# Optimization experiments

Measured on AMD Instinct MI355X. Metric: run time of the kernel, lower is better.

The kernel has to match this reference:

```python
import jax, jax.numpy as jnp
import numpy as np
from jax import lax

VOCAB = 32000
H = 1024
T = 4096


def setup_inputs() -> dict:
    key = jax.random.key(0)
    ks = jax.random.split(key, 6)
    s = 1.0 / np.sqrt(H)  # PyTorch GRU init scale
    x = jax.random.randint(ks[0], (T,), 0, VOCAB)
    embedding = jax.random.normal(ks[1], (VOCAB, H), dtype=jnp.float32)
    # direction 0 = 'forward', direction 1 = 'reverse' (both run left-to-right
    # here because the original feeds one timestep at a time)
    w_ih = jax.random.uniform(ks[2], (2, 3 * H, H), jnp.float32, -s, s)
    w_hh = jax.random.uniform(ks[3], (2, 3 * H, H), jnp.float32, -s, s)
    b_ih = jax.random.uniform(ks[4], (2, 3 * H), jnp.float32, -s, s)
    b_hh = jax.random.uniform(ks[5], (2, 3 * H), jnp.float32, -s, s)
    return {"x": x, "embedding": embedding, "w_ih": w_ih, "w_hh": w_hh,
            "b_ih": b_ih, "b_hh": b_hh}


def reference(x, embedding, w_ih, w_hh, b_ih, b_hh):
    emb = embedding[x]  # (T, H)
    # Precompute input-side gate projections for both directions: (T, 2, 3H)
    x_proj = jnp.einsum('th,dgh->tdg', emb, w_ih) + b_ih

    def step(h, xp):  # h: (2, H), xp: (2, 3H)
        hp = jnp.einsum('dh,dgh->dg', h, w_hh) + b_hh  # (2, 3H)
        xr, xz, xn = xp[:, :H], xp[:, H:2 * H], xp[:, 2 * H:]
        hr, hz, hn = hp[:, :H], hp[:, H:2 * H], hp[:, 2 * H:]
        r = jax.nn.sigmoid(xr + hr)
        z = jax.nn.sigmoid(xz + hz)
        n = jnp.tanh(xn + r * hn)
        h_new = (1.0 - z) * n + z * h
        return h_new, h_new

    h0 = jnp.zeros((2, H), emb.dtype)
    h_last, hs = lax.scan(step, h0, x_proj)  # hs: (T, 2, H)
    # per-step output = concat(dir0_hidden, dir1_hidden) -> (T, 2H)
    outputs = hs.reshape(T, 2 * H)
    # final hidden = sum of the two direction hiddens, shape (1, H)
    hidden = (h_last[0] + h_last[1])[None, :]
    return outputs, hidden
```

## Files before the change

kernel.cpp:

```cpp
#include <hip/hip_runtime.h>
#include <hip/hip_bf16.h>
#include <stdint.h>

#define HDIM 1024
#define TSEQ 4096
#define GATES3 3072
#define NTOT 6144

#define COMM_OFF (64u * 1024 * 1024)
#define XFIN_OFF (COMM_OFF + 32768)

typedef __attribute__((ext_vector_type(8))) short short8;
typedef __attribute__((ext_vector_type(4))) float f32x4;
typedef __attribute__((ext_vector_type(4))) unsigned int ux4;

__device__ __forceinline__ unsigned short f2bf(float f) {
    uint32_t u = __float_as_uint(f);
    uint32_t r = (u + 0x7FFFu + ((u >> 16) & 1u)) >> 16;
    return (unsigned short)r;
}
__device__ __forceinline__ float bf2f(unsigned short s) {
    return __uint_as_float(((uint32_t)s) << 16);
}

__device__ __forceinline__ ux4 ld16_agent(const void* p) {
    ux4 r;
    asm volatile("global_load_dwordx4 %0, %1, off sc1\n\ts_waitcnt vmcnt(0)"
                 : "=v"(r) : "v"(p) : "memory");
    return r;
}
__device__ __forceinline__ ux4 ld16_sys(const void* p) {
    ux4 r;
    asm volatile("global_load_dwordx4 %0, %1, off sc0 sc1\n\ts_waitcnt vmcnt(0)"
                 : "=v"(r) : "v"(p) : "memory");
    return r;
}

__global__ __launch_bounds__(256) void init_comm_kernel(uint8_t* __restrict__ wsb) {
    int i = blockIdx.x * 256 + threadIdx.x;
    unsigned long long* comm = (unsigned long long*)(wsb + COMM_OFF);
    unsigned long long* xfin = (unsigned long long*)(wsb + XFIN_OFF);
    if (i < 4096) comm[i] = ~0ull;
    if (i < 1024) xfin[i] = ~0ull;
}

__global__ __launch_bounds__(256) void xproj_gemm_kernel(
    const int* __restrict__ x, const float* __restrict__ emb,
    const float* __restrict__ w_ih, const float* __restrict__ b_ih,
    unsigned short* __restrict__ rz, float* __restrict__ n32)
{
    __shared__ short As[128][32];
    __shared__ short Bs[128][32];

    const int tid = threadIdx.x;
    const int m0 = blockIdx.x * 128;
    const int n0 = blockIdx.y * 128;

    const int srow = tid >> 1;
    const int half = tid & 1;

    const int arow_g = x[m0 + srow];
    const float* aptr = emb + (size_t)arow_g * HDIM + half * 16;
    const float* bptr = w_ih + (size_t)(n0 + srow) * HDIM + half * 16;

    const int wid = tid >> 6;
    const int lane = tid & 63;
    const int wm = wid >> 1;
    const int wn = wid & 1;
    const int l15 = lane & 15;
    const int ksel = (lane >> 4) * 8;

    f32x4 acc[4][4];
    f32x4 zero4 = {0.f, 0.f, 0.f, 0.f};
#pragma unroll
    for (int mi = 0; mi < 4; mi++)
#pragma unroll
        for (int ni = 0; ni < 4; ni++) acc[mi][ni] = zero4;

    for (int k0 = 0; k0 < HDIM; k0 += 32) {
        float4 av[4], bv[4];
#pragma unroll
        for (int jj = 0; jj < 4; jj++) {
            av[jj] = *(const float4*)(aptr + k0 + jj * 4);
            bv[jj] = *(const float4*)(bptr + k0 + jj * 4);
        }
        if (k0) __syncthreads();
        short ta[16], tb[16];
#pragma unroll
        for (int jj = 0; jj < 4; jj++) {
            ta[jj*4+0] = f2bf(av[jj].x); ta[jj*4+1] = f2bf(av[jj].y);
            ta[jj*4+2] = f2bf(av[jj].z); ta[jj*4+3] = f2bf(av[jj].w);
            tb[jj*4+0] = f2bf(bv[jj].x); tb[jj*4+1] = f2bf(bv[jj].y);
            tb[jj*4+2] = f2bf(bv[jj].z); tb[jj*4+3] = f2bf(bv[jj].w);
        }
        *(short8*)&As[srow][half * 16]     = *(short8*)&ta[0];
        *(short8*)&As[srow][half * 16 + 8] = *(short8*)&ta[8];
        *(short8*)&Bs[srow][half * 16]     = *(short8*)&tb[0];
        *(short8*)&Bs[srow][half * 16 + 8] = *(short8*)&tb[8];
        __syncthreads();

        short8 af[4], bfr[4];
#pragma unroll
        for (int mi = 0; mi < 4; mi++)
            af[mi] = *(const short8*)&As[wm * 64 + mi * 16 + l15][ksel];
#pragma unroll
        for (int ni = 0; ni < 4; ni++)
            bfr[ni] = *(const short8*)&Bs[wn * 64 + ni * 16 + l15][ksel];
#pragma unroll
        for (int mi = 0; mi < 4; mi++)
#pragma unroll
            for (int ni = 0; ni < 4; ni++)
                acc[mi][ni] = __builtin_amdgcn_mfma_f32_16x16x32_bf16(
                    af[mi], bfr[ni], acc[mi][ni], 0, 0, 0);
    }

    const int r0 = m0 + wm * 64;
    const int c0 = n0 + wn * 64;
#pragma unroll
    for (int mi = 0; mi < 4; mi++) {
#pragma unroll
        for (int ni = 0; ni < 4; ni++) {
            int c = c0 + ni * 16 + l15;
            int dir = (c >= GATES3) ? 1 : 0;
            int g3 = c - dir * GATES3;
            int gate = g3 >> 10;
            int jj = g3 & 1023;
            float bias = b_ih[c];
#pragma unroll
            for (int v = 0; v < 4; v++) {
                int r = r0 + mi * 16 + (lane >> 4) * 4 + v;
                float val = acc[mi][ni][v] + bias;
                if (gate < 2)
                    rz[(size_t)r * 4096 + dir * 2048 + gate * 1024 + jj] = f2bf(val);
                else
                    n32[(size_t)r * 2048 + dir * 1024 + jj] = val;
            }
        }
    }
}

__global__ __launch_bounds__(512, 1) void rnn_kernel(
    const unsigned short* __restrict__ rz, const float* __restrict__ n32,
    const float* __restrict__ w_hh, const float* __restrict__ b_hh,
    uint8_t* __restrict__ wsb, float* __restrict__ out)
{
    __shared__ float h_lds[2][1152];

    uint8_t* comm = wsb + COMM_OFF;
    unsigned long long* xfin = (unsigned long long*)(wsb + XFIN_OFF);

    const int tid = threadIdx.x;
    const int bid = blockIdx.x;
    const int dir = bid >> 6;
    const int role = bid & 63;
    const int g   = tid >> 5;
    const int sl  = tid & 31;
    const int j   = role * 16 + g;

    f32x4 w0[8], w1[8], w2[8];
    {
        const float* Wd = w_hh + (size_t)dir * GATES3 * HDIM;
        const float* p0 = Wd + ((size_t)(0 * HDIM + j)) * HDIM + sl * 32;
        const float* p1 = Wd + ((size_t)(1 * HDIM + j)) * HDIM + sl * 32;
        const float* p2 = Wd + ((size_t)(2 * HDIM + j)) * HDIM + sl * 32;
#pragma unroll
        for (int c4 = 0; c4 < 8; c4++) {
            w0[c4] = *(const f32x4*)(p0 + c4 * 4);
            w1[c4] = *(const f32x4*)(p1 + c4 * 4);
            w2[c4] = *(const f32x4*)(p2 + c4 * 4);
        }
    }
    float bh0 = 0.f, bh1 = 0.f, bh2 = 0.f;
    if (sl == 0) {
        bh0 = b_hh[dir * GATES3 + j];
        bh1 = b_hh[dir * GATES3 + HDIM + j];
        bh2 = b_hh[dir * GATES3 + 2 * HDIM + j];
    }

    uint8_t* commD = comm + dir * 8192;
    const uint8_t* poll0 = commD + (size_t)tid * 16;
    const uint8_t* poll1 = poll0 + 16384;
    unsigned long long* slot0 = (unsigned long long*)(commD) + j;
    unsigned long long* slot1 = (unsigned long long*)(commD + 16384) + j;

    const int idx0 = (tid >> 4) * 36 + 2 * (tid & 15);
    const int jidx = (j >> 5) * 36 + (j & 31);
    const unsigned short* rzp = rz + dir * 2048 + j;
    const float* np = n32 + dir * 1024 + j;
    const int ocol = role * 16 + 2 * tid;
    const int oidx = (ocol >> 5) * 36 + (ocol & 31);

    float last_h = 0.f;

    for (int t = 0; t < TSEQ; t++) {
        const int buf = t & 1;

        float xr = 0.f, xz = 0.f, xn = 0.f;
        if (sl == 0) {
            xr = bf2f(rzp[0]);
            xz = bf2f(rzp[1024]);
            xn = np[0];
        }
        rzp += 4096; np += 2048;

        if (t == 0) {
            h_lds[0][idx0]     = 0.f;
            h_lds[0][idx0 + 1] = 0.f;
        } else {
            const uint32_t want = (uint32_t)(t - 1);
            const uint8_t* src = ((t - 1) & 1) ? poll1 : poll0;
            ux4 v;
            int spins = 0;
            for (;;) {
                v = ld16_agent(src);
                if (v.x == want && v.z == want) break;
                if (++spins > 4096) {
                    v = ld16_sys(src);
                    if (v.x == want && v.z == want) break;
                }
            }
            h_lds[buf][idx0]     = __uint_as_float(v.y);
            h_lds[buf][idx0 + 1] = __uint_as_float(v.w);
        }
        __syncthreads();

        if (t > 0 && tid < 8) {
            float2 hv = *(float2*)&h_lds[buf][oidx];
            *(float2*)(out + (size_t)(t - 1) * 2048 + dir * 1024 + ocol) = hv;
        }

        f32x4 s0 = {0,0,0,0}, s1 = {0,0,0,0}, s2 = {0,0,0,0};
        const float* hb = &h_lds[buf][sl * 36];
#pragma unroll
        for (int c4 = 0; c4 < 8; c4++) {
            f32x4 hv = *(const f32x4*)(hb + c4 * 4);
            s0 += w0[c4] * hv;
            s1 += w1[c4] * hv;
            s2 += w2[c4] * hv;
        }
        float a0 = s0.x + s0.y + s0.z + s0.w;
        float a1 = s1.x + s1.y + s1.z + s1.w;
        float a2 = s2.x + s2.y + s2.z + s2.w;
#pragma unroll
        for (int m = 1; m < 32; m <<= 1) {
            a0 += __shfl_xor(a0, m, 32);
            a1 += __shfl_xor(a1, m, 32);
            a2 += __shfl_xor(a2, m, 32);
        }

        if (sl == 0) {
            float r  = 1.f / (1.f + __expf(-(xr + a0 + bh0)));
            float z  = 1.f / (1.f + __expf(-(xz + a1 + bh1)));
            float y  = xn + r * (a2 + bh2);
            float e2 = __expf(2.f * y);
            float n_ = 1.f - 2.f / (e2 + 1.f);
            float hp = h_lds[buf][jidx];
            float hnew = z * (hp - n_) + n_;
            last_h = hnew;
            unsigned long long pack =
                ((unsigned long long)__float_as_uint(hnew) << 32) | (uint32_t)t;
            __hip_atomic_store((t & 1) ? slot1 : slot0, pack,
                               __ATOMIC_RELAXED, __HIP_MEMORY_SCOPE_AGENT);
        }
    }

    if (sl == 0)
        out[(size_t)(TSEQ - 1) * 2048 + dir * 1024 + j] = last_h;

    if (dir == 1 && sl == 0) {
        unsigned long long pack =
            ((unsigned long long)__float_as_uint(last_h) << 32) | 0x0BADF00Du;
        __hip_atomic_store(&xfin[j], pack, __ATOMIC_RELAXED, __HIP_MEMORY_SCOPE_AGENT);
    }
    if (dir == 0 && sl == 0) {
        unsigned long long v;
        do {
            v = __hip_atomic_load(&xfin[j], __ATOMIC_RELAXED, __HIP_MEMORY_SCOPE_AGENT);
        } while ((uint32_t)v != 0x0BADF00Du);
        out[(size_t)TSEQ * 2048 + j] = last_h + __uint_as_float((uint32_t)(v >> 32));
    }
}

extern "C" void kernel_launch(void* const* d_in, const int* in_sizes, int n_in,
                              void* d_out, int out_size, void* d_ws, size_t ws_size,
                              hipStream_t stream)
{
    const int*   x     = (const int*)d_in[0];
    const float* emb   = (const float*)d_in[1];
    const float* w_ih  = (const float*)d_in[2];
    const float* w_hh  = (const float*)d_in[3];
    const float* b_ih  = (const float*)d_in[4];
    const float* b_hh  = (const float*)d_in[5];
    float* out = (float*)d_out;

    unsigned short* rz  = (unsigned short*)d_ws;
    float* n32 = (float*)((char*)d_ws + (size_t)TSEQ * 4096 * 2);
    uint8_t* wsb = (uint8_t*)d_ws;

    init_comm_kernel<<<16, 256, 0, stream>>>(wsb);

    dim3 g(TSEQ / 128, NTOT / 128);
    xproj_gemm_kernel<<<g, 256, 0, stream>>>(x, emb, w_ih, b_ih, rz, n32);

    const unsigned short* a0 = rz;
    const float* a1 = n32;
    const float* a2 = w_hh;
    const float* a3 = b_hh;
    uint8_t* a4 = wsb;
    float* a5 = out;
    void* args[] = { (void*)&a0, (void*)&a1, (void*)&a2, (void*)&a3, (void*)&a4, (void*)&a5 };
    hipLaunchCooperativeKernel((void*)rnn_kernel, dim3(128), dim3(512), args, 0, stream);
}
```

Before: 7.188 ms.

## Prefetch next-step input projections and write outputs from the owning lane

Loads the next timestep's input-gate projections after the barrier so their global latency overlaps the matvec, instead of issuing them at the top of each step on the critical path. The previous hidden value is now kept in a register rather than re-read from LDS. Each output element is written directly by its owning lane at compute time, replacing the separate copy of the gathered vector out of LDS. The spin threshold before falling back to system-scope loads is raised, which makes the costlier load rarer but can delay recovery if agent-scope loads stay stale.

```diff
diff --git a/kernel.cpp b/kernel.cpp
--- a/kernel.cpp
+++ b/kernel.cpp
@@ -13,6 +13,7 @@
 typedef __attribute__((ext_vector_type(8))) short short8;
 typedef __attribute__((ext_vector_type(4))) float f32x4;
 typedef __attribute__((ext_vector_type(4))) unsigned int ux4;
+typedef unsigned long long u64;
 
 __device__ __forceinline__ unsigned short f2bf(float f) {
     uint32_t u = __float_as_uint(f);
@@ -38,8 +39,8 @@
 
 __global__ __launch_bounds__(256) void init_comm_kernel(uint8_t* __restrict__ wsb) {
     int i = blockIdx.x * 256 + threadIdx.x;
-    unsigned long long* comm = (unsigned long long*)(wsb + COMM_OFF);
-    unsigned long long* xfin = (unsigned long long*)(wsb + XFIN_OFF);
+    u64* comm = (u64*)(wsb + COMM_OFF);
+    u64* xfin = (u64*)(wsb + XFIN_OFF);
     if (i < 4096) comm[i] = ~0ull;
     if (i < 1024) xfin[i] = ~0ull;
 }
@@ -147,7 +148,7 @@
     __shared__ float h_lds[2][1152];
 
     uint8_t* comm = wsb + COMM_OFF;
-    unsigned long long* xfin = (unsigned long long*)(wsb + XFIN_OFF);
+    u64* xfin = (u64*)(wsb + XFIN_OFF);
 
     const int tid = threadIdx.x;
     const int bid = blockIdx.x;
@@ -180,28 +181,25 @@
     uint8_t* commD = comm + dir * 8192;
     const uint8_t* poll0 = commD + (size_t)tid * 16;
     const uint8_t* poll1 = poll0 + 16384;
-    unsigned long long* slot0 = (unsigned long long*)(commD) + j;
-    unsigned long long* slot1 = (unsigned long long*)(commD + 16384) + j;
+    u64* slot0 = (u64*)(commD) + j;
+    u64* slot1 = (u64*)(commD + 16384) + j;
 
     const int idx0 = (tid >> 4) * 36 + 2 * (tid & 15);
-    const int jidx = (j >> 5) * 36 + (j & 31);
     const unsigned short* rzp = rz + dir * 2048 + j;
     const float* np = n32 + dir * 1024 + j;
-    const int ocol = role * 16 + 2 * tid;
-    const int oidx = (ocol >> 5) * 36 + (ocol & 31);
 
     float last_h = 0.f;
+
+    float xr = 0.f, xz = 0.f, xn = 0.f;
+    if (sl == 0) {
+        xr = bf2f(rzp[0]);
+        xz = bf2f(rzp[1024]);
+        xn = np[0];
+    }
+    rzp += 4096; np += 2048;
 
     for (int t = 0; t < TSEQ; t++) {
         const int buf = t & 1;
-
-        float xr = 0.f, xz = 0.f, xn = 0.f;
-        if (sl == 0) {
-            xr = bf2f(rzp[0]);
-            xz = bf2f(rzp[1024]);
-            xn = np[0];
-        }
-        rzp += 4096; np += 2048;
 
         if (t == 0) {
             h_lds[0][idx0]     = 0.f;
@@ -214,9 +212,10 @@
             for (;;) {
                 v = ld16_agent(src);
                 if (v.x == want && v.z == want) break;
-                if (++spins > 4096) {
+                if (++spins > (1 << 16)) {
                     v = ld16_sys(src);
                     if (v.x == want && v.z == want) break;
+                    spins = (1 << 15);
                 }
             }
             h_lds[buf][idx0]     = __uint_as_float(v.y);
@@ -224,10 +223,13 @@
         }
         __syncthreads();
 
-        if (t > 0 && tid < 8) {
-            float2 hv = *(float2*)&h_lds[buf][oidx];
-            *(float2*)(out + (size_t)(t - 1) * 2048 + dir * 1024 + ocol) = hv;
-        }
+        float nxr = 0.f, nxz = 0.f, nxn = 0.f;
+        if (sl == 0) {
+            nxr = bf2f(rzp[0]);
+            nxz = bf2f(rzp[1024]);
+            nxn = np[0];
+        }
+        rzp += 4096; np += 2048;
 
         f32x4 s0 = {0,0,0,0}, s1 = {0,0,0,0}, s2 = {0,0,0,0};
         const float* hb = &h_lds[buf][sl * 36];
@@ -254,26 +256,22 @@
             float y  = xn + r * (a2 + bh2);
             float e2 = __expf(2.f * y);
             float n_ = 1.f - 2.f / (e2 + 1.f);
-            float hp = h_lds[buf][jidx];
-            float hnew = z * (hp - n_) + n_;
+            float hnew = z * (last_h - n_) + n_;
             last_h = hnew;
-            unsigned long long pack =
-                ((unsigned long long)__float_as_uint(hnew) << 32) | (uint32_t)t;
+            u64 pack = ((u64)__float_as_uint(hnew) << 32) | (uint32_t)t;
             __hip_atomic_store((t & 1) ? slot1 : slot0, pack,
                                __ATOMIC_RELAXED, __HIP_MEMORY_SCOPE_AGENT);
-        }
-    }
-
-    if (sl == 0)
-        out[(size_t)(TSEQ - 1) * 2048 + dir * 1024 + j] = last_h;
+            out[(size_t)t * 2048 + dir * 1024 + j] = hnew;
+        }
+        xr = nxr; xz = nxz; xn = nxn;
+    }
 
     if (dir == 1 && sl == 0) {
-        unsigned long long pack =
-            ((unsigned long long)__float_as_uint(last_h) << 32) | 0x0BADF00Du;
+        u64 pack = ((u64)__float_as_uint(last_h) << 32) | 0x0BADF00Du;
         __hip_atomic_store(&xfin[j], pack, __ATOMIC_RELAXED, __HIP_MEMORY_SCOPE_AGENT);
     }
     if (dir == 0 && sl == 0) {
-        unsigned long long v;
+        u64 v;
         do {
             v = __hip_atomic_load(&xfin[j], __ATOMIC_RELAXED, __HIP_MEMORY_SCOPE_AGENT);
         } while ((uint32_t)v != 0x0BADF00Du);
```

Result: slower. 12.31 ms (+71.2%).
